# Optimization experiments

Hardware: AMD Instinct MI355X
Metric: run time of the kernel (lower is better)

## Reference

```python
import jax, jax.numpy as jnp
import numpy as np

N = 100_000      # nodes
E = 1_600_000    # edges
B = 256          # graphs
DIM = 64
EPS = 1e-5


def _batchnorm(h, gamma, beta):
    # BatchNorm1d in training mode: batch mean, biased variance
    mu = jnp.mean(h, axis=0)
    var = jnp.mean((h - mu) ** 2, axis=0)
    return (h - mu) * jax.lax.rsqrt(var + EPS) * gamma + beta


def setup_inputs() -> dict:
    key = jax.random.key(0)
    ks = jax.random.split(key, 12)
    x = jax.random.normal(ks[0], (N, DIM), dtype=jnp.float32)
    edge_index = jax.random.randint(ks[1], (2, E), 0, N, dtype=jnp.int64)
    edge_attr = jax.random.normal(ks[2], (E, DIM), dtype=jnp.float32)
    state = jax.random.normal(ks[3], (B, DIM), dtype=jnp.float32)
    batch = jnp.sort(jax.random.randint(ks[4], (N,), 0, B, dtype=jnp.int64))
    s = 0.05
    params = {
        "W1": jax.random.normal(ks[5], (DIM, 3 * DIM), dtype=jnp.float32) * s,
        "b1": jnp.zeros((DIM,), jnp.float32),
        "g1": jnp.ones((DIM,), jnp.float32),
        "be1": jnp.zeros((DIM,), jnp.float32),
        "W2": jax.random.normal(ks[6], (DIM, DIM), dtype=jnp.float32) * s,
        "b2": jnp.zeros((DIM,), jnp.float32),
        "g2": jnp.ones((DIM,), jnp.float32),
        "be2": jnp.zeros((DIM,), jnp.float32),
        "W3": jax.random.normal(ks[7], (DIM, DIM), dtype=jnp.float32) * s,
        "b3": jnp.zeros((DIM,), jnp.float32),
        "g3": jnp.ones((DIM,), jnp.float32),
        "be3": jnp.zeros((DIM,), jnp.float32),
    }
    return {"x": x, "edge_index": edge_index, "edge_attr": edge_attr,
            "state": state, "batch": batch, **params}


def reference(x, edge_index, edge_attr, state, batch,
              W1, b1, g1, be1, W2, b2, g2, be2, W3, b3, g3, be3):
    n = x.shape[0]
    src = edge_index[0]
    # scatter-mean of edge_attr onto destination-of-src nodes
    sums = jax.ops.segment_sum(edge_attr, src, num_segments=n)
    cnt = jax.ops.segment_sum(jnp.ones((edge_attr.shape[0],), edge_attr.dtype),
                              src, num_segments=n)
    v_mean = sums / jnp.maximum(cnt, 1.0)[:, None]
    comb = jnp.concatenate([x, v_mean, state[batch]], axis=1)  # [N, 3*DIM]
    h = jax.nn.relu(comb @ W1.T + b1)
    h = _batchnorm(h, g1, be1)
    h = jax.nn.relu(h @ W2.T + b2)
    h = _batchnorm(h, g2, be2)
    h = h @ W3.T + b3
    return _batchnorm(h, g3, be3)
```

## Files before the change

kernel.cpp:

```cpp
#include <hip/hip_runtime.h>

#define NN 100000
#define NE 1600000
#define EPSV 1e-5f
#define NTILE 1563

typedef float f32x4 __attribute__((ext_vector_type(4)));
typedef short s16x8 __attribute__((ext_vector_type(8)));

__device__ __forceinline__ unsigned short f2bf(float f) {
  unsigned int u = __float_as_uint(f);
  u += 0x7fffu + ((u >> 16) & 1u);
  return (unsigned short)(u >> 16);
}

__device__ __forceinline__ float bf2f(unsigned short s) {
  return __uint_as_float(((unsigned int)s) << 16);
}

__device__ __forceinline__ ushort4 pack4(float4 v) {
  ushort4 s;
  s.x = f2bf(v.x); s.y = f2bf(v.y); s.z = f2bf(v.z); s.w = f2bf(v.w);
  return s;
}

__global__ __launch_bounds__(256) void k_bucket_g1a(
    const int* __restrict__ ei, int* __restrict__ cnt, int* __restrict__ eids,
    const float4* __restrict__ x4, const float4* __restrict__ state4,
    const int* __restrict__ batch, const float4* __restrict__ w14,
    f32x4* __restrict__ ph) {
  __shared__ unsigned short lx[64][136];
  __shared__ unsigned short lw[64][136];
  const int idx = blockIdx.x;
  const int tid = threadIdx.x;
  const bool is_g1a = ((idx % 5) == 2) && (idx / 5 < NTILE);
  if (!is_g1a) {
    int nga = idx / 5 + (((idx % 5) > 2) ? 1 : 0);
    if (nga > NTILE) nga = NTILE;
    int e = (idx - nga) * 256 + tid;
    int src = ei[e];
    int pos = atomicAdd(&cnt[src], 1);
    if (pos < 64) eids[(size_t)src * 64 + pos] = e;
    return;
  }
  const int tile = idx / 5;
  const int nodeBase = tile * 64;
#pragma unroll
  for (int i = 0; i < 4; ++i) {
    int t = tid + i * 256;
    int j = t >> 4, q = t & 15;
    *(ushort4*)&lw[j][q * 4]      = pack4(w14[j * 48 + q]);
    *(ushort4*)&lw[j][64 + q * 4] = pack4(w14[j * 48 + 32 + q]);
  }
#pragma unroll
  for (int i = 0; i < 4; ++i) {
    int t = tid + i * 256;
    int node = t >> 4, q = t & 15;
    int g = nodeBase + node;
    float4 vx = {0,0,0,0}, vs = {0,0,0,0};
    if (g < NN) {
      vx = x4[(size_t)g * 16 + q];
      vs = state4[batch[g] * 16 + q];
    }
    *(ushort4*)&lx[node][q * 4]      = pack4(vx);
    *(ushort4*)&lx[node][64 + q * 4] = pack4(vs);
  }
  __syncthreads();
  const int lane = tid & 63, w = tid >> 6;
  const int rg = lane >> 4, ci = lane & 15;
  f32x4 acc[4] = {{0,0,0,0},{0,0,0,0},{0,0,0,0},{0,0,0,0}};
#pragma unroll
  for (int s = 0; s < 4; ++s) {
    int k0 = 32 * s + rg * 8;
    s16x8 a = *(const s16x8*)&lx[w * 16 + ci][k0];
#pragma unroll
    for (int c = 0; c < 4; ++c) {
      s16x8 b = *(const s16x8*)&lw[c * 16 + ci][k0];
      acc[c] = __builtin_amdgcn_mfma_f32_16x16x32_bf16(a, b, acc[c], 0, 0, 0);
    }
  }
#pragma unroll
  for (int c = 0; c < 4; ++c)
    ph[(size_t)tile * 1024 + tid * 4 + c] = acc[c];
}

__global__ __launch_bounds__(256) void k_gather(
    const int* __restrict__ cnt, const int* __restrict__ eids,
    const float4* __restrict__ ea4, ushort4* __restrict__ vmb4) {
  int wid = (blockIdx.x * 256 + threadIdx.x) >> 6;
  int lane = threadIdx.x & 63;
  int grp = lane >> 4, q = lane & 15;
  int n0 = wid * 13;
  int nend = n0 + 13 < NN ? n0 + 13 : NN;
  for (int n = n0; n < nend; ++n) {
    const int* elist = eids + (size_t)n * 64;
    int c = cnt[n];
    int m = c < 64 ? c : 64;
    int rm = m - 1;
    float ax = 0.f, ay = 0.f, az = 0.f, aw = 0.f;
    {
      int r0 = grp,      r1 = 4 + grp,  r2 = 8 + grp,  r3 = 12 + grp;
      int r4 = 16 + grp, r5 = 20 + grp, r6 = 24 + grp, r7 = 28 + grp;
      int i0 = elist[r0 < m ? r0 : rm];
      int i1 = elist[r1 < m ? r1 : rm];
      int i2 = elist[r2 < m ? r2 : rm];
      int i3 = elist[r3 < m ? r3 : rm];
      int i4 = elist[r4 < m ? r4 : rm];
      int i5 = elist[r5 < m ? r5 : rm];
      int i6 = elist[r6 < m ? r6 : rm];
      int i7 = elist[r7 < m ? r7 : rm];
      float4 v0 = ea4[(size_t)i0 * 16 + q];
      float4 v1 = ea4[(size_t)i1 * 16 + q];
      float4 v2 = ea4[(size_t)i2 * 16 + q];
      float4 v3 = ea4[(size_t)i3 * 16 + q];
      float4 v4 = ea4[(size_t)i4 * 16 + q];
      float4 v5 = ea4[(size_t)i5 * 16 + q];
      float4 v6 = ea4[(size_t)i6 * 16 + q];
      float4 v7 = ea4[(size_t)i7 * 16 + q];
      float m0 = r0 < m ? 1.f : 0.f, m1 = r1 < m ? 1.f : 0.f;
      float m2 = r2 < m ? 1.f : 0.f, m3 = r3 < m ? 1.f : 0.f;
      ax += m0 * v0.x + m1 * v1.x + m2 * v2.x + m3 * v3.x;
      ay += m0 * v0.y + m1 * v1.y + m2 * v2.y + m3 * v3.y;
      az += m0 * v0.z + m1 * v1.z + m2 * v2.z + m3 * v3.z;
      aw += m0 * v0.w + m1 * v1.w + m2 * v2.w + m3 * v3.w;
      float m4 = r4 < m ? 1.f : 0.f, m5 = r5 < m ? 1.f : 0.f;
      float m6 = r6 < m ? 1.f : 0.f, m7 = r7 < m ? 1.f : 0.f;
      ax += m4 * v4.x + m5 * v5.x + m6 * v6.x + m7 * v7.x;
      ay += m4 * v4.y + m5 * v5.y + m6 * v6.y + m7 * v7.y;
      az += m4 * v4.z + m5 * v5.z + m6 * v6.z + m7 * v7.z;
      aw += m4 * v4.w + m5 * v5.w + m6 * v6.w + m7 * v7.w;
    }
    if (m > 32) {
      for (int e = 32; e < m; e += 16) {
        int r0 = e + grp, r1 = e + 4 + grp, r2 = e + 8 + grp, r3 = e + 12 + grp;
        int i0 = elist[r0 < m ? r0 : rm];
        int i1 = elist[r1 < m ? r1 : rm];
        int i2 = elist[r2 < m ? r2 : rm];
        int i3 = elist[r3 < m ? r3 : rm];
        float4 v0 = ea4[(size_t)i0 * 16 + q];
        float4 v1 = ea4[(size_t)i1 * 16 + q];
        float4 v2 = ea4[(size_t)i2 * 16 + q];
        float4 v3 = ea4[(size_t)i3 * 16 + q];
        float m0 = r0 < m ? 1.f : 0.f, m1 = r1 < m ? 1.f : 0.f;
        float m2 = r2 < m ? 1.f : 0.f, m3 = r3 < m ? 1.f : 0.f;
        ax += m0 * v0.x + m1 * v1.x + m2 * v2.x + m3 * v3.x;
        ay += m0 * v0.y + m1 * v1.y + m2 * v2.y + m3 * v3.y;
        az += m0 * v0.z + m1 * v1.z + m2 * v2.z + m3 * v3.z;
        aw += m0 * v0.w + m1 * v1.w + m2 * v2.w + m3 * v3.w;
      }
    }
    ax += __shfl_xor(ax, 16); ay += __shfl_xor(ay, 16);
    az += __shfl_xor(az, 16); aw += __shfl_xor(aw, 16);
    ax += __shfl_xor(ax, 32); ay += __shfl_xor(ay, 32);
    az += __shfl_xor(az, 32); aw += __shfl_xor(aw, 32);
    if (lane < 16) {
      float inv = 1.0f / fmaxf((float)c, 1.0f);
      float4 r; r.x = ax * inv; r.y = ay * inv; r.z = az * inv; r.w = aw * inv;
      vmb4[(size_t)n * 16 + lane] = pack4(r);
    }
  }
}

__global__ __launch_bounds__(256) void k_g1b(
    const ushort4* __restrict__ vmb4, const float4* __restrict__ w14,
    const float* __restrict__ b1, const f32x4* __restrict__ ph,
    unsigned short* __restrict__ h1,
    float* __restrict__ Sout, float* __restrict__ Qout) {
  __shared__ unsigned short lv[64][72];
  __shared__ unsigned short lwv[64][72];
  __shared__ float ssum[64], ssq[64];
  const int tid = threadIdx.x;
  const int tile = blockIdx.x;
  const int nodeBase = tile * 64;
  if (tid < 64) { ssum[tid] = 0.f; ssq[tid] = 0.f; }
#pragma unroll
  for (int i = 0; i < 4; ++i) {
    int t = tid + i * 256;
    int j = t >> 4, q = t & 15;
    *(ushort4*)&lwv[j][q * 4] = pack4(w14[j * 48 + 16 + q]);
    int g = nodeBase + j;
    ushort4 vm = {0,0,0,0};
    if (g < NN) vm = vmb4[(size_t)g * 16 + q];
    *(ushort4*)&lv[j][q * 4] = vm;
  }
  __syncthreads();
  const int lane = tid & 63, w = tid >> 6;
  const int rg = lane >> 4, ci = lane & 15;
  f32x4 acc[4];
#pragma unroll
  for (int c = 0; c < 4; ++c) acc[c] = ph[(size_t)tile * 1024 + tid * 4 + c];
#pragma unroll
  for (int s = 0; s < 2; ++s) {
    int k0 = 32 * s + rg * 8;
    s16x8 a = *(const s16x8*)&lv[w * 16 + ci][k0];
#pragma unroll
    for (int c = 0; c < 4; ++c) {
      s16x8 b = *(const s16x8*)&lwv[c * 16 + ci][k0];
      acc[c] = __builtin_amdgcn_mfma_f32_16x16x32_bf16(a, b, acc[c], 0, 0, 0);
    }
  }
  __syncthreads();
  unsigned short (*lo)[72] = (unsigned short(*)[72])lwv;
#pragma unroll
  for (int c = 0; c < 4; ++c) {
    int col = c * 16 + ci;
    float bb = b1[col];
    float ls = 0.f, lq = 0.f;
#pragma unroll
    for (int r = 0; r < 4; ++r) {
      int row = w * 16 + rg * 4 + r;
      float v = fmaxf(acc[c][r] + bb, 0.f);
      lo[row][col] = f2bf(v);
      if (nodeBase + row < NN) { ls += v; lq += v * v; }
    }
    atomicAdd(&ssum[col], ls);
    atomicAdd(&ssq[col], lq);
  }
  __syncthreads();
#pragma unroll
  for (int i = 0; i < 2; ++i) {
    int t = tid + i * 256;
    int row = t >> 3, q = t & 7;
    int g = nodeBase + row;
    if (g < NN) *(s16x8*)&h1[(size_t)g * 64 + q * 8] = *(const s16x8*)&lo[row][q * 8];
  }
  if (tid < 64) {
    unsafeAtomicAdd(&Sout[tid], ssum[tid]);
    unsafeAtomicAdd(&Qout[tid], ssq[tid]);
  }
}

template <bool RELU>
__global__ __launch_bounds__(256) void k_gemm64f(
    const s16x8* __restrict__ A8,
    const float* __restrict__ Wf,
    const float* __restrict__ bias,
    const float* __restrict__ gm, const float* __restrict__ bt,
    const float* __restrict__ Sin, const float* __restrict__ Qin,
    unsigned short* __restrict__ Obf,
    float* __restrict__ Sout, float* __restrict__ Qout) {
  __shared__ unsigned short la[64][72];
  __shared__ unsigned short lwf[64][72];
  __shared__ float lA[64], lC[64], ld[64], red[256], ssum[64], ssq[64];
  const int tid = threadIdx.x;
  const int nodeBase = blockIdx.x * 64;
  if (tid < 64) {
    float mu = Sin[tid] * (1.0f / NN);
    float var = Qin[tid] * (1.0f / NN) - mu * mu;
    float a = gm[tid] * rsqrtf(var + EPSV);
    lA[tid] = a; lC[tid] = bt[tid] - mu * a;
    ssum[tid] = 0.f; ssq[tid] = 0.f;
  }
  __syncthreads();
#pragma unroll
  for (int i = 0; i < 2; ++i) {
    int t = tid + i * 256;
    int row = t >> 3, q = t & 7;
    int g = nodeBase + row;
    s16x8 v = {};
    if (g < NN) v = A8[(size_t)g * 8 + q];
    *(s16x8*)&la[row][q * 8] = v;
  }
#pragma unroll
  for (int i = 0; i < 16; ++i) {
    int t = tid + i * 256;
    lwf[t >> 6][t & 63] = f2bf(Wf[t] * lA[t & 63]);
  }
  {
    int j = tid >> 2, p = tid & 3;
    const float* Wr = Wf + j * 64 + p * 16;
    float s = 0.f;
#pragma unroll
    for (int k = 0; k < 16; ++k) s += lC[p * 16 + k] * Wr[k];
    red[tid] = s;
  }
  __syncthreads();
  if (tid < 64) ld[tid] = bias[tid] + red[tid*4] + red[tid*4+1] + red[tid*4+2] + red[tid*4+3];
  __syncthreads();
  const int lane = tid & 63, w = tid >> 6;
  const int rg = lane >> 4, ci = lane & 15;
  f32x4 acc[4] = {{0,0,0,0},{0,0,0,0},{0,0,0,0},{0,0,0,0}};
#pragma unroll
  for (int s = 0; s < 2; ++s) {
    int k0 = 32 * s + rg * 8;
    s16x8 a = *(const s16x8*)&la[w * 16 + ci][k0];
#pragma unroll
    for (int c = 0; c < 4; ++c) {
      s16x8 b = *(const s16x8*)&lwf[c * 16 + ci][k0];
      acc[c] = __builtin_amdgcn_mfma_f32_16x16x32_bf16(a, b, acc[c], 0, 0, 0);
    }
  }
  __syncthreads();
  unsigned short (*lo)[72] = (unsigned short(*)[72])la;
#pragma unroll
  for (int c = 0; c < 4; ++c) {
    int col = c * 16 + ci;
    float dd = ld[col];
    float ls = 0.f, lq = 0.f;
#pragma unroll
    for (int r = 0; r < 4; ++r) {
      int row = w * 16 + rg * 4 + r;
      float v = acc[c][r] + dd;
      if (RELU) v = fmaxf(v, 0.f);
      lo[row][col] = f2bf(v);
      if (nodeBase + row < NN) { ls += v; lq += v * v; }
    }
    atomicAdd(&ssum[col], ls);
    atomicAdd(&ssq[col], lq);
  }
  __syncthreads();
#pragma unroll
  for (int i = 0; i < 2; ++i) {
    int t = tid + i * 256;
    int row = t >> 3, q = t & 7;
    int g = nodeBase + row;
    if (g < NN) *(s16x8*)&Obf[(size_t)g * 64 + q * 8] = *(const s16x8*)&lo[row][q * 8];
  }
  if (tid < 64) {
    unsafeAtomicAdd(&Sout[tid], ssum[tid]);
    unsafeAtomicAdd(&Qout[tid], ssq[tid]);
  }
}

__global__ __launch_bounds__(256) void k_bn3(
    const s16x8* __restrict__ h3b, const float* __restrict__ gm,
    const float* __restrict__ bt, const float* __restrict__ S,
    const float* __restrict__ Q, float4* __restrict__ out) {
  __shared__ float lA[64], lC[64];
  const int tid = threadIdx.x;
  if (tid < 64) {
    float mu = S[tid] * (1.0f / NN);
    float var = Q[tid] * (1.0f / NN) - mu * mu;
    float a = gm[tid] * rsqrtf(var + EPSV);
    lA[tid] = a;
    lC[tid] = bt[tid] - mu * a;
  }
  __syncthreads();
  const int total = NN * 8;
  for (int idx = blockIdx.x * 256 + tid; idx < total; idx += gridDim.x * 256) {
    s16x8 v = h3b[idx];
    int k = (idx & 7) * 8;
    float4 o0, o1;
    o0.x = bf2f((unsigned short)v[0]) * lA[k]     + lC[k];
    o0.y = bf2f((unsigned short)v[1]) * lA[k + 1] + lC[k + 1];
    o0.z = bf2f((unsigned short)v[2]) * lA[k + 2] + lC[k + 2];
    o0.w = bf2f((unsigned short)v[3]) * lA[k + 3] + lC[k + 3];
    o1.x = bf2f((unsigned short)v[4]) * lA[k + 4] + lC[k + 4];
    o1.y = bf2f((unsigned short)v[5]) * lA[k + 5] + lC[k + 5];
    o1.z = bf2f((unsigned short)v[6]) * lA[k + 6] + lC[k + 6];
    o1.w = bf2f((unsigned short)v[7]) * lA[k + 7] + lC[k + 7];
    out[idx * 2]     = o0;
    out[idx * 2 + 1] = o1;
  }
}

extern "C" void kernel_launch(void* const* d_in, const int* in_sizes, int n_in,
                              void* d_out, int out_size, void* d_ws, size_t ws_size,
                              hipStream_t stream) {
  const float* x     = (const float*)d_in[0];
  const int*   ei    = (const int*)d_in[1];
  const float* ea    = (const float*)d_in[2];
  const float* state = (const float*)d_in[3];
  const int*   batch = (const int*)d_in[4];
  const float* W1  = (const float*)d_in[5];
  const float* b1  = (const float*)d_in[6];
  const float* g1  = (const float*)d_in[7];
  const float* be1 = (const float*)d_in[8];
  const float* W2  = (const float*)d_in[9];
  const float* b2  = (const float*)d_in[10];
  const float* g2  = (const float*)d_in[11];
  const float* be2 = (const float*)d_in[12];
  const float* W3  = (const float*)d_in[13];
  const float* b3  = (const float*)d_in[14];
  const float* g3  = (const float*)d_in[15];
  const float* be3 = (const float*)d_in[16];

  char* ws = (char*)d_ws;
  int*   cnt  = (int*)ws;
  float* S1   = (float*)(ws + 400000);
  float* Q1 = S1 + 64;
  float* S2 = S1 + 128;
  float* Q2 = S1 + 192;
  float* S3 = S1 + 256;
  float* Q3 = S1 + 320;
  int*            eids = (int*)(ws + 401536);
  unsigned short* h3b  = (unsigned short*)(ws + 401536);
  unsigned short* vmb  = (unsigned short*)(ws + 26018432);
  unsigned short* h2   = (unsigned short*)(ws + 26018432);
  unsigned short* h1   = (unsigned short*)(ws + 38818432);
  f32x4*          ph   = (f32x4*)(ws + 51618432);

  hipMemsetAsync(ws, 0, 401536, stream);

  k_bucket_g1a<<<6250 + NTILE, 256, 0, stream>>>(
      ei, cnt, eids, (const float4*)x, (const float4*)state, batch,
      (const float4*)W1, ph);
  k_gather<<<2048, 256, 0, stream>>>(cnt, eids, (const float4*)ea, (ushort4*)vmb);
  k_g1b<<<NTILE, 256, 0, stream>>>((const ushort4*)vmb, (const float4*)W1,
                                   b1, ph, h1, S1, Q1);
  k_gemm64f<true><<<NTILE, 256, 0, stream>>>(
      (const s16x8*)h1, W2, b2, g1, be1, S1, Q1, h2, S2, Q2);
  k_gemm64f<false><<<NTILE, 256, 0, stream>>>(
      (const s16x8*)h2, W3, b3, g2, be2, S2, Q2, h3b, S3, Q3);
  k_bn3<<<2048, 256, 0, stream>>>((const s16x8*)h3b, g3, be3, S3, Q3, (float4*)d_out);
}
```

Before: 363.8 us.

## Replace bucketed edge-id gather with CSR scatter of bf16 edge features

```diff
diff --git a/kernel.cpp b/kernel.cpp
--- a/kernel.cpp
+++ b/kernel.cpp
@@ -24,8 +24,8 @@
   return s;
 }
 
-__global__ __launch_bounds__(256) void k_bucket_g1a(
-    const int* __restrict__ ei, int* __restrict__ cnt, int* __restrict__ eids,
+__global__ __launch_bounds__(256) void k_hist_g1a(
+    const int* __restrict__ ei, int* __restrict__ cnt,
     const float4* __restrict__ x4, const float4* __restrict__ state4,
     const int* __restrict__ batch, const float4* __restrict__ w14,
     f32x4* __restrict__ ph) {
@@ -38,9 +38,7 @@
     int nga = idx / 5 + (((idx % 5) > 2) ? 1 : 0);
     if (nga > NTILE) nga = NTILE;
     int e = (idx - nga) * 256 + tid;
-    int src = ei[e];
-    int pos = atomicAdd(&cnt[src], 1);
-    if (pos < 64) eids[(size_t)src * 64 + pos] = e;
+    atomicAdd(&cnt[ei[e]], 1);
     return;
   }
   const int tile = idx / 5;
@@ -84,87 +82,75 @@
     ph[(size_t)tile * 1024 + tid * 4 + c] = acc[c];
 }
 
-__global__ __launch_bounds__(256) void k_gather(
-    const int* __restrict__ cnt, const int* __restrict__ eids,
-    const float4* __restrict__ ea4, ushort4* __restrict__ vmb4) {
-  int wid = (blockIdx.x * 256 + threadIdx.x) >> 6;
-  int lane = threadIdx.x & 63;
-  int grp = lane >> 4, q = lane & 15;
-  int n0 = wid * 13;
-  int nend = n0 + 13 < NN ? n0 + 13 : NN;
-  for (int n = n0; n < nend; ++n) {
-    const int* elist = eids + (size_t)n * 64;
-    int c = cnt[n];
-    int m = c < 64 ? c : 64;
-    int rm = m - 1;
-    float ax = 0.f, ay = 0.f, az = 0.f, aw = 0.f;
-    {
-      int r0 = grp,      r1 = 4 + grp,  r2 = 8 + grp,  r3 = 12 + grp;
-      int r4 = 16 + grp, r5 = 20 + grp, r6 = 24 + grp, r7 = 28 + grp;
-      int i0 = elist[r0 < m ? r0 : rm];
-      int i1 = elist[r1 < m ? r1 : rm];
-      int i2 = elist[r2 < m ? r2 : rm];
-      int i3 = elist[r3 < m ? r3 : rm];
-      int i4 = elist[r4 < m ? r4 : rm];
-      int i5 = elist[r5 < m ? r5 : rm];
-      int i6 = elist[r6 < m ? r6 : rm];
-      int i7 = elist[r7 < m ? r7 : rm];
-      float4 v0 = ea4[(size_t)i0 * 16 + q];
-      float4 v1 = ea4[(size_t)i1 * 16 + q];
-      float4 v2 = ea4[(size_t)i2 * 16 + q];
-      float4 v3 = ea4[(size_t)i3 * 16 + q];
-      float4 v4 = ea4[(size_t)i4 * 16 + q];
-      float4 v5 = ea4[(size_t)i5 * 16 + q];
-      float4 v6 = ea4[(size_t)i6 * 16 + q];
-      float4 v7 = ea4[(size_t)i7 * 16 + q];
-      float m0 = r0 < m ? 1.f : 0.f, m1 = r1 < m ? 1.f : 0.f;
-      float m2 = r2 < m ? 1.f : 0.f, m3 = r3 < m ? 1.f : 0.f;
-      ax += m0 * v0.x + m1 * v1.x + m2 * v2.x + m3 * v3.x;
-      ay += m0 * v0.y + m1 * v1.y + m2 * v2.y + m3 * v3.y;
-      az += m0 * v0.z + m1 * v1.z + m2 * v2.z + m3 * v3.z;
-      aw += m0 * v0.w + m1 * v1.w + m2 * v2.w + m3 * v3.w;
-      float m4 = r4 < m ? 1.f : 0.f, m5 = r5 < m ? 1.f : 0.f;
-      float m6 = r6 < m ? 1.f : 0.f, m7 = r7 < m ? 1.f : 0.f;
-      ax += m4 * v4.x + m5 * v5.x + m6 * v6.x + m7 * v7.x;
-      ay += m4 * v4.y + m5 * v5.y + m6 * v6.y + m7 * v7.y;
-      az += m4 * v4.z + m5 * v5.z + m6 * v6.z + m7 * v7.z;
-      aw += m4 * v4.w + m5 * v5.w + m6 * v6.w + m7 * v7.w;
-    }
-    if (m > 32) {
-      for (int e = 32; e < m; e += 16) {
-        int r0 = e + grp, r1 = e + 4 + grp, r2 = e + 8 + grp, r3 = e + 12 + grp;
-        int i0 = elist[r0 < m ? r0 : rm];
-        int i1 = elist[r1 < m ? r1 : rm];
-        int i2 = elist[r2 < m ? r2 : rm];
-        int i3 = elist[r3 < m ? r3 : rm];
-        float4 v0 = ea4[(size_t)i0 * 16 + q];
-        float4 v1 = ea4[(size_t)i1 * 16 + q];
-        float4 v2 = ea4[(size_t)i2 * 16 + q];
-        float4 v3 = ea4[(size_t)i3 * 16 + q];
-        float m0 = r0 < m ? 1.f : 0.f, m1 = r1 < m ? 1.f : 0.f;
-        float m2 = r2 < m ? 1.f : 0.f, m3 = r3 < m ? 1.f : 0.f;
-        ax += m0 * v0.x + m1 * v1.x + m2 * v2.x + m3 * v3.x;
-        ay += m0 * v0.y + m1 * v1.y + m2 * v2.y + m3 * v3.y;
-        az += m0 * v0.z + m1 * v1.z + m2 * v2.z + m3 * v3.z;
-        aw += m0 * v0.w + m1 * v1.w + m2 * v2.w + m3 * v3.w;
-      }
-    }
-    ax += __shfl_xor(ax, 16); ay += __shfl_xor(ay, 16);
-    az += __shfl_xor(az, 16); aw += __shfl_xor(aw, 16);
-    ax += __shfl_xor(ax, 32); ay += __shfl_xor(ay, 32);
-    az += __shfl_xor(az, 32); aw += __shfl_xor(aw, 32);
-    if (lane < 16) {
-      float inv = 1.0f / fmaxf((float)c, 1.0f);
-      float4 r; r.x = ax * inv; r.y = ay * inv; r.z = az * inv; r.w = aw * inv;
-      vmb4[(size_t)n * 16 + lane] = pack4(r);
-    }
-  }
-}
-
-__global__ __launch_bounds__(256) void k_g1b(
-    const ushort4* __restrict__ vmb4, const float4* __restrict__ w14,
-    const float* __restrict__ b1, const f32x4* __restrict__ ph,
-    unsigned short* __restrict__ h1,
+__global__ __launch_bounds__(1024) void k_scan(
+    const int* __restrict__ cnt, int* __restrict__ csr, int* __restrict__ cur) {
+  __shared__ int part[1024];
+  const int t = threadIdx.x;
+  const int base = t * 98;
+  int s = 0;
+  for (int i = 0; i < 98; ++i) {
+    int n = base + i;
+    if (n < NN) s += cnt[n];
+  }
+  part[t] = s;
+  __syncthreads();
+  for (int off = 1; off < 1024; off <<= 1) {
+    int v = (t >= off) ? part[t - off] : 0;
+    __syncthreads();
+    part[t] += v;
+    __syncthreads();
+  }
+  int run = (t == 0) ? 0 : part[t - 1];
+  for (int i = 0; i < 98; ++i) {
+    int n = base + i;
+    if (n < NN) {
+      csr[n] = run;
+      cur[n] = run;
+      run += cnt[n];
+    }
+  }
+  if (t == 1023) csr[NN] = run;
+}
+
+__global__ __launch_bounds__(256) void k_scat(
+    const int* __restrict__ ei, int* __restrict__ cur,
+    const float2* __restrict__ ea2, unsigned int* __restrict__ eab) {
+  const int gid = blockIdx.x * 256 + threadIdx.x;
+  const int hw = gid >> 5;
+  const int sub = gid & 31;
+  const int lane = threadIdx.x & 63;
+  const size_t e0 = (size_t)hw * 98;
+  for (int j = 0; j < 98; j += 4) {
+    size_t e = e0 + j;
+    bool g0 =                 (e     < NE);
+    bool g1 = (j + 1 < 98) && (e + 1 < NE);
+    bool g2 = (j + 2 < 98) && (e + 2 < NE);
+    bool g3 = (j + 3 < 98) && (e + 3 < NE);
+    int p = 0;
+    if (sub < 4) {
+      size_t ee = e + sub;
+      if ((j + sub < 98) && (ee < NE)) p = atomicAdd(&cur[ei[ee]], 1);
+    }
+    float2 d0 = {0,0}, d1 = {0,0}, d2 = {0,0}, d3 = {0,0};
+    if (g0) d0 = ea2[(e + 0) * 32 + sub];
+    if (g1) d1 = ea2[(e + 1) * 32 + sub];
+    if (g2) d2 = ea2[(e + 2) * 32 + sub];
+    if (g3) d3 = ea2[(e + 3) * 32 + sub];
+    int p0 = __shfl(p, (lane & 32) + 0);
+    int p1 = __shfl(p, (lane & 32) + 1);
+    int p2 = __shfl(p, (lane & 32) + 2);
+    int p3 = __shfl(p, (lane & 32) + 3);
+    if (g0) eab[(size_t)p0 * 32 + sub] = ((unsigned int)f2bf(d0.y) << 16) | f2bf(d0.x);
+    if (g1) eab[(size_t)p1 * 32 + sub] = ((unsigned int)f2bf(d1.y) << 16) | f2bf(d1.x);
+    if (g2) eab[(size_t)p2 * 32 + sub] = ((unsigned int)f2bf(d2.y) << 16) | f2bf(d2.x);
+    if (g3) eab[(size_t)p3 * 32 + sub] = ((unsigned int)f2bf(d3.y) << 16) | f2bf(d3.x);
+  }
+}
+
+__global__ __launch_bounds__(256) void k_g2b(
+    const int* __restrict__ csr, const unsigned int* __restrict__ eab,
+    const float4* __restrict__ w14, const float* __restrict__ b1,
+    const f32x4* __restrict__ ph, unsigned short* __restrict__ h1,
     float* __restrict__ Sout, float* __restrict__ Qout) {
   __shared__ unsigned short lv[64][72];
   __shared__ unsigned short lwv[64][72];
@@ -178,38 +164,68 @@
     int t = tid + i * 256;
     int j = t >> 4, q = t & 15;
     *(ushort4*)&lwv[j][q * 4] = pack4(w14[j * 48 + 16 + q]);
-    int g = nodeBase + j;
-    ushort4 vm = {0,0,0,0};
-    if (g < NN) vm = vmb4[(size_t)g * 16 + q];
-    *(ushort4*)&lv[j][q * 4] = vm;
-  }
-  __syncthreads();
+  }
   const int lane = tid & 63, w = tid >> 6;
+  const int half = lane >> 5, c = lane & 31;
+  for (int k = 0; k < 16; ++k) {
+    int n = nodeBase + w * 16 + k;
+    float a0 = 0.f, a1 = 0.f;
+    int deg = 0;
+    if (n < NN) {
+      int r0 = csr[n], r1 = csr[n + 1];
+      deg = r1 - r0;
+      const unsigned int* base = eab + (size_t)r0 * 32 + c;
+      int r = half;
+      for (; r + 6 < deg; r += 8) {
+        unsigned int u0 = base[(size_t)(r)     * 32];
+        unsigned int u1 = base[(size_t)(r + 2) * 32];
+        unsigned int u2 = base[(size_t)(r + 4) * 32];
+        unsigned int u3 = base[(size_t)(r + 6) * 32];
+        a0 += bf2f((unsigned short)(u0 & 0xffff)) + bf2f((unsigned short)(u1 & 0xffff))
+            + bf2f((unsigned short)(u2 & 0xffff)) + bf2f((unsigned short)(u3 & 0xffff));
+        a1 += bf2f((unsigned short)(u0 >> 16)) + bf2f((unsigned short)(u1 >> 16))
+            + bf2f((unsigned short)(u2 >> 16)) + bf2f((unsigned short)(u3 >> 16));
+      }
+      for (; r < deg; r += 2) {
+        unsigned int u = base[(size_t)r * 32];
+        a0 += bf2f((unsigned short)(u & 0xffff));
+        a1 += bf2f((unsigned short)(u >> 16));
+      }
+    }
+    a0 += __shfl_xor(a0, 32);
+    a1 += __shfl_xor(a1, 32);
+    if (half == 0) {
+      float inv = 1.0f / fmaxf((float)deg, 1.0f);
+      unsigned int pk = ((unsigned int)f2bf(a1 * inv) << 16) | f2bf(a0 * inv);
+      *(unsigned int*)&lv[w * 16 + k][c * 2] = pk;
+    }
+  }
+  __syncthreads();
   const int rg = lane >> 4, ci = lane & 15;
   f32x4 acc[4];
 #pragma unroll
-  for (int c = 0; c < 4; ++c) acc[c] = ph[(size_t)tile * 1024 + tid * 4 + c];
+  for (int cc = 0; cc < 4; ++cc) acc[cc] = ph[(size_t)tile * 1024 + tid * 4 + cc];
 #pragma unroll
   for (int s = 0; s < 2; ++s) {
     int k0 = 32 * s + rg * 8;
     s16x8 a = *(const s16x8*)&lv[w * 16 + ci][k0];
 #pragma unroll
-    for (int c = 0; c < 4; ++c) {
-      s16x8 b = *(const s16x8*)&lwv[c * 16 + ci][k0];
-      acc[c] = __builtin_amdgcn_mfma_f32_16x16x32_bf16(a, b, acc[c], 0, 0, 0);
+    for (int cc = 0; cc < 4; ++cc) {
+      s16x8 b = *(const s16x8*)&lwv[cc * 16 + ci][k0];
+      acc[cc] = __builtin_amdgcn_mfma_f32_16x16x32_bf16(a, b, acc[cc], 0, 0, 0);
     }
   }
   __syncthreads();
   unsigned short (*lo)[72] = (unsigned short(*)[72])lwv;
 #pragma unroll
-  for (int c = 0; c < 4; ++c) {
-    int col = c * 16 + ci;
+  for (int cc = 0; cc < 4; ++cc) {
+    int col = cc * 16 + ci;
     float bb = b1[col];
     float ls = 0.f, lq = 0.f;
 #pragma unroll
     for (int r = 0; r < 4; ++r) {
       int row = w * 16 + rg * 4 + r;
-      float v = fmaxf(acc[c][r] + bb, 0.f);
+      float v = fmaxf(acc[cc][r] + bb, 0.f);
       lo[row][col] = f2bf(v);
       if (nodeBase + row < NN) { ls += v; lq += v * v; }
     }
@@ -383,21 +399,23 @@
   float* Q2 = S1 + 192;
   float* S3 = S1 + 256;
   float* Q3 = S1 + 320;
-  int*            eids = (int*)(ws + 401536);
-  unsigned short* h3b  = (unsigned short*)(ws + 401536);
-  unsigned short* vmb  = (unsigned short*)(ws + 26018432);
-  unsigned short* h2   = (unsigned short*)(ws + 26018432);
-  unsigned short* h1   = (unsigned short*)(ws + 38818432);
-  f32x4*          ph   = (f32x4*)(ws + 51618432);
+  int*            csr = (int*)(ws + 401536);
+  int*            cur = (int*)(ws + 801792);
+  f32x4*          ph  = (f32x4*)(ws + 1202048);
+  unsigned short* h1  = (unsigned short*)(ws + 26810240);
+  unsigned short* h2  = (unsigned short*)(ws + 39610240);
+  unsigned short* h3b = (unsigned short*)(ws + 52410240);
+  unsigned int*   eab = (unsigned int*)(ws + 65210240);
 
   hipMemsetAsync(ws, 0, 401536, stream);
 
-  k_bucket_g1a<<<6250 + NTILE, 256, 0, stream>>>(
-      ei, cnt, eids, (const float4*)x, (const float4*)state, batch,
+  k_hist_g1a<<<6250 + NTILE, 256, 0, stream>>>(
+      ei, cnt, (const float4*)x, (const float4*)state, batch,
       (const float4*)W1, ph);
-  k_gather<<<2048, 256, 0, stream>>>(cnt, eids, (const float4*)ea, (ushort4*)vmb);
-  k_g1b<<<NTILE, 256, 0, stream>>>((const ushort4*)vmb, (const float4*)W1,
-                                   b1, ph, h1, S1, Q1);
+  k_scan<<<1, 1024, 0, stream>>>(cnt, csr, cur);
+  k_scat<<<2048, 256, 0, stream>>>(ei, cur, (const float2*)ea, eab);
+  k_g2b<<<NTILE, 256, 0, stream>>>(csr, eab, (const float4*)W1, b1, ph,
+                                   h1, S1, Q1);
   k_gemm64f<true><<<NTILE, 256, 0, stream>>>(
       (const s16x8*)h1, W2, b2, g1, be1, S1, Q1, h2, S2, Q2);
   k_gemm64f<false><<<NTILE, 256, 0, stream>>>(
```

After: 676.4 us. 85.9% more time.
